# Optimization experiments

Measured on AMD Instinct MI355X. Metric: run time of the kernel, lower is better.

The kernel has to match this reference:

```python
import jax, jax.numpy as jnp
import numpy as np

N_FRUSTUMS = 14400  # n_splits_azi(360) * n_splits_pol(40)
N_POINTS = 2_000_000
N_CHANNELS = 8


def setup_inputs() -> dict:
    key = jax.random.key(0)
    k1, k2 = jax.random.split(key)
    pc = jax.random.normal(k1, (N_POINTS, N_CHANNELS), dtype=jnp.float32)
    i_frustum = jnp.sort(
        jax.random.randint(k2, (N_POINTS,), 0, N_FRUSTUMS)
    ).astype(jnp.int32)
    i_inv = jnp.arange(N_POINTS, dtype=jnp.int32)  # identity inverse permutation
    counts_padded = jnp.bincount(i_frustum, length=N_FRUSTUMS).astype(jnp.float32)
    return {
        "pc": pc,
        "i_frustum": i_frustum,
        "i_inv": i_inv,
        "counts_padded": counts_padded,
    }


def reference(pc, i_frustum, i_inv, counts_padded):
    """Faithful port of symmetrize_mean / symmetrize_std / symmetrize_max plus the
    gather-broadcast normalize (pc - mean[i_frustum][i_inv]) / std.

    pc:            [N, C] float point features
    i_frustum:     [N]   int point->frustum segment ids (sorted)
    i_inv:         [N]   int inverse permutation applied after gather
    counts_padded: [F]   float per-frustum point counts (0 for empty frustums)
    """
    n_frustums = counts_padded.shape[0]
    nonempty = counts_padded[:, None] != 0.0  # [F, 1]
    safe_counts = jnp.maximum(counts_padded, 1.0)[:, None]  # avoid div-by-zero

    # symmetrize_mean: scatter_add then divide where count != 0
    sums = jax.ops.segment_sum(pc, i_frustum, num_segments=n_frustums)  # [F, C]
    mean = jnp.where(nonempty, sums / safe_counts, sums)

    # symmetrize_std: scatter_add of squared deviation, divide, sqrt where > 0
    dev = pc - mean[i_frustum][i_inv]  # [N, C] gather-broadcast subtract
    var_sums = jax.ops.segment_sum(dev * dev, i_frustum, num_segments=n_frustums)
    var = jnp.where(nonempty, var_sums / safe_counts, var_sums)
    std = jnp.where(var > 0.0, jnp.sqrt(jnp.maximum(var, 0.0)), var)

    # symmetrize_max: scatter_reduce amax onto a zeros-initialized buffer
    # (include_self=True default in torch => result is max(0, segment max))
    frustum_max = jnp.zeros((n_frustums, pc.shape[1]), pc.dtype).at[i_frustum].max(pc)

    # gather-broadcast normalize (decorator_distance_to_mean style, with per-frustum std)
    std_g = std[i_frustum][i_inv]
    pc_norm = dev / jnp.where(std_g > 0.0, std_g, 1.0)

    return mean, std, frustum_max, pc_norm
```

## Files before the change

### kernel.cpp

```cpp
#include <hip/hip_runtime.h>

#define NCH 8
#define CACHE 8

typedef float v4f __attribute__((ext_vector_type(4)));

__device__ __forceinline__ int lower_bound_i32(const int* __restrict__ a, int n, int key) {
    int lo = 0, hi = n;
    while (lo < hi) {
        int mid = (lo + hi) >> 1;
        if (a[mid] < key) lo = mid + 1; else hi = mid;
    }
    return lo;
}

__global__ __launch_bounds__(256) void k_starts(const int* __restrict__ i_frustum, int n, int F,
                                                int* __restrict__ starts) {
    int t = blockIdx.x * blockDim.x + threadIdx.x;
    if (t <= F) starts[t] = lower_bound_i32(i_frustum, n, t);
}

__device__ __forceinline__ void acc4(const float4& v, float4& sum, float4& sq, float4& mx) {
    sum.x += v.x; sq.x += v.x * v.x; mx.x = fmaxf(mx.x, v.x);
    sum.y += v.y; sq.y += v.y * v.y; mx.y = fmaxf(mx.y, v.y);
    sum.z += v.z; sq.z += v.z * v.z; mx.z = fmaxf(mx.z, v.z);
    sum.w += v.w; sq.w += v.w * v.w; mx.w = fmaxf(mx.w, v.w);
}

__device__ __forceinline__ v4f norm4(const float4& v, const float4& m, const float4& d) {
    v4f o;
    o.x = (v.x - m.x) * d.x;
    o.y = (v.y - m.y) * d.y;
    o.z = (v.z - m.z) * d.z;
    o.w = (v.w - m.w) * d.w;
    return o;
}

__global__ __launch_bounds__(128) void k_wave(
    const float* __restrict__ pc, const float* __restrict__ counts,
    const int* __restrict__ starts, int F,
    float* __restrict__ out_mean, float* __restrict__ out_std,
    float* __restrict__ out_max, float* __restrict__ out_pcn)
{
    const int wid = (blockIdx.x * blockDim.x + threadIdx.x) >> 6;
    if (wid >= F) return;
    const int lane = threadIdx.x & 63;

    const int s = starts[wid];
    const int e = starts[wid + 1];
    const float4* __restrict__ pc4 = reinterpret_cast<const float4*>(pc);
    v4f* __restrict__ out4 = reinterpret_cast<v4f*>(out_pcn);

    const int b = s * 2, E = e * 2;

    float4 sum = {0.f, 0.f, 0.f, 0.f};
    float4 sq  = {0.f, 0.f, 0.f, 0.f};
    float4 mx  = {0.f, 0.f, 0.f, 0.f};
    float4 c[CACHE];

    int k = b + lane;
    #pragma unroll
    for (int u = 0; u < CACHE; ++u) {
        if (k < E) { c[u] = pc4[k]; acc4(c[u], sum, sq, mx); }
        k += 64;
    }
    for (int kk = k; kk < E; kk += 64) { float4 v = pc4[kk]; acc4(v, sum, sq, mx); }

    #pragma unroll
    for (int m = 2; m <= 32; m <<= 1) {
        sum.x += __shfl_xor(sum.x, m, 64);
        sum.y += __shfl_xor(sum.y, m, 64);
        sum.z += __shfl_xor(sum.z, m, 64);
        sum.w += __shfl_xor(sum.w, m, 64);
        sq.x  += __shfl_xor(sq.x,  m, 64);
        sq.y  += __shfl_xor(sq.y,  m, 64);
        sq.z  += __shfl_xor(sq.z,  m, 64);
        sq.w  += __shfl_xor(sq.w,  m, 64);
        mx.x = fmaxf(mx.x, __shfl_xor(mx.x, m, 64));
        mx.y = fmaxf(mx.y, __shfl_xor(mx.y, m, 64));
        mx.z = fmaxf(mx.z, __shfl_xor(mx.z, m, 64));
        mx.w = fmaxf(mx.w, __shfl_xor(mx.w, m, 64));
    }

    const float cnt  = counts[wid];
    const float invc = 1.0f / fmaxf(cnt, 1.0f);
    float4 mean, sd, dv;
    mean.x = sum.x * invc; mean.y = sum.y * invc; mean.z = sum.z * invc; mean.w = sum.w * invc;
    float vx = fmaxf(sq.x * invc - mean.x * mean.x, 0.0f);
    float vy = fmaxf(sq.y * invc - mean.y * mean.y, 0.0f);
    float vz = fmaxf(sq.z * invc - mean.z * mean.z, 0.0f);
    float vw = fmaxf(sq.w * invc - mean.w * mean.w, 0.0f);
    sd.x = sqrtf(vx); sd.y = sqrtf(vy); sd.z = sqrtf(vz); sd.w = sqrtf(vw);
    dv.x = 1.0f / (sd.x > 0.f ? sd.x : 1.f);
    dv.y = 1.0f / (sd.y > 0.f ? sd.y : 1.f);
    dv.z = 1.0f / (sd.z > 0.f ? sd.z : 1.f);
    dv.w = 1.0f / (sd.w > 0.f ? sd.w : 1.f);

    if (lane < 2) {
        reinterpret_cast<float4*>(out_mean + (size_t)wid * NCH)[lane] = mean;
        reinterpret_cast<float4*>(out_std  + (size_t)wid * NCH)[lane] = sd;
        reinterpret_cast<float4*>(out_max  + (size_t)wid * NCH)[lane] = mx;
    }

    k = b + lane;
    #pragma unroll
    for (int u = 0; u < CACHE; ++u) {
        if (k < E) {
            v4f o = norm4(c[u], mean, dv);
            __builtin_nontemporal_store(o, &out4[k]);
        }
        k += 64;
    }
    for (int kk = k; kk < E; kk += 64) {
        v4f o = norm4(pc4[kk], mean, dv);
        __builtin_nontemporal_store(o, &out4[kk]);
    }
}

extern "C" void kernel_launch(void* const* d_in, const int* in_sizes, int n_in,
                              void* d_out, int out_size, void* d_ws, size_t ws_size,
                              hipStream_t stream) {
    const float* pc        = (const float*)d_in[0];
    const int*   i_frustum = (const int*)d_in[1];
    const float* counts    = (const float*)d_in[3];

    int n = in_sizes[0] / NCH;
    int F = in_sizes[3];

    float* out_mean = (float*)d_out;
    float* out_std  = out_mean + (size_t)F * NCH;
    float* out_max  = out_std  + (size_t)F * NCH;
    float* out_pcn  = out_max  + (size_t)F * NCH;

    int* starts = (int*)d_ws;

    k_starts<<<(F + 1 + 255) / 256, 256, 0, stream>>>(i_frustum, n, F, starts);
    int waves_per_block = 128 / 64;
    int blocks = (F + waves_per_block - 1) / waves_per_block;
    k_wave<<<blocks, 128, 0, stream>>>(pc, counts, starts, F, out_mean, out_std, out_max, out_pcn);
}
```

Baseline: 34.70 us.

## Fuse segment-start search into main kernel with wave-cooperative 64-ary search

Removes the separate k_starts launch and the starts workspace. Each wave now finds its segment start with a 64-way cooperative search that uses ballot and popcount, taking about log64(N) rounds of loads. The segment end is taken as start plus counts[wid], so only one search is needed per wave. This saves a kernel launch and the dependency between the two kernels, at the cost of a few dependent global-memory rounds at the start of every wave.

```diff
diff --git a/kernel.cpp b/kernel.cpp
--- a/kernel.cpp
+++ b/kernel.cpp
@@ -4,21 +4,6 @@
 #define CACHE 8
 
 typedef float v4f __attribute__((ext_vector_type(4)));
-
-__device__ __forceinline__ int lower_bound_i32(const int* __restrict__ a, int n, int key) {
-    int lo = 0, hi = n;
-    while (lo < hi) {
-        int mid = (lo + hi) >> 1;
-        if (a[mid] < key) lo = mid + 1; else hi = mid;
-    }
-    return lo;
-}
-
-__global__ __launch_bounds__(256) void k_starts(const int* __restrict__ i_frustum, int n, int F,
-                                                int* __restrict__ starts) {
-    int t = blockIdx.x * blockDim.x + threadIdx.x;
-    if (t <= F) starts[t] = lower_bound_i32(i_frustum, n, t);
-}
 
 __device__ __forceinline__ void acc4(const float4& v, float4& sum, float4& sq, float4& mx) {
     sum.x += v.x; sq.x += v.x * v.x; mx.x = fmaxf(mx.x, v.x);
@@ -36,9 +21,30 @@
     return o;
 }
 
-__global__ __launch_bounds__(128) void k_wave(
-    const float* __restrict__ pc, const float* __restrict__ counts,
-    const int* __restrict__ starts, int F,
+__device__ __forceinline__ int wave_lower_bound(const int* __restrict__ a, int n, int key,
+                                                int lane) {
+    int lo = 0, len = n;
+    while (len > 64) {
+        int step = (len + 63) >> 6;
+        int p = lo + lane * step;
+        int v = (p < lo + len) ? a[p] : 0x7fffffff;
+        unsigned long long bal = __ballot(v < key);
+        int cnt = __popcll(bal);
+        if (cnt == 0) return lo;
+        int nlo = lo + (cnt - 1) * step + 1;
+        int nhi = lo + len;
+        int cap = lo + cnt * step;
+        if (cnt < 64 && cap < nhi) nhi = cap;
+        lo = nlo; len = nhi - nlo;
+    }
+    int v = (lane < len) ? a[lo + lane] : 0x7fffffff;
+    unsigned long long bal = __ballot(v < key);
+    return lo + __popcll(bal);
+}
+
+__global__ __launch_bounds__(128) void k_fused(
+    const float* __restrict__ pc, const int* __restrict__ i_frustum,
+    const float* __restrict__ counts, int n, int F,
     float* __restrict__ out_mean, float* __restrict__ out_std,
     float* __restrict__ out_max, float* __restrict__ out_pcn)
 {
@@ -46,8 +52,10 @@
     if (wid >= F) return;
     const int lane = threadIdx.x & 63;
 
-    const int s = starts[wid];
-    const int e = starts[wid + 1];
+    const int s = wave_lower_bound(i_frustum, n, wid, lane);
+    const float cnt = counts[wid];
+    const int e = s + (int)cnt;
+
     const float4* __restrict__ pc4 = reinterpret_cast<const float4*>(pc);
     v4f* __restrict__ out4 = reinterpret_cast<v4f*>(out_pcn);
 
@@ -82,7 +90,6 @@
         mx.w = fmaxf(mx.w, __shfl_xor(mx.w, m, 64));
     }
 
-    const float cnt  = counts[wid];
     const float invc = 1.0f / fmaxf(cnt, 1.0f);
     float4 mean, sd, dv;
     mean.x = sum.x * invc; mean.y = sum.y * invc; mean.z = sum.z * invc; mean.w = sum.w * invc;
@@ -132,10 +139,8 @@
     float* out_max  = out_std  + (size_t)F * NCH;
     float* out_pcn  = out_max  + (size_t)F * NCH;
 
-    int* starts = (int*)d_ws;
-
-    k_starts<<<(F + 1 + 255) / 256, 256, 0, stream>>>(i_frustum, n, F, starts);
     int waves_per_block = 128 / 64;
     int blocks = (F + waves_per_block - 1) / waves_per_block;
-    k_wave<<<blocks, 128, 0, stream>>>(pc, counts, starts, F, out_mean, out_std, out_max, out_pcn);
+    k_fused<<<blocks, 128, 0, stream>>>(pc, i_frustum, counts, n, F,
+                                        out_mean, out_std, out_max, out_pcn);
 }
```

New measurement: 31.50 us. 9.2% less time.
